# Kernel tuning notes

Measured on AMD Instinct MI355X. Metric: run time of the kernel, lower is better.

The kernel has to match this reference:

```python
import jax, jax.numpy as jnp
import numpy as np

B, T, D_IN, H, D_OUT = 64, 512, 256, 512, 1


def _lstm_layer(x, w_ih, w_hh, b_ih, b_hh):
    """PyTorch-convention LSTM layer. x: [B,T,Din]; w_ih: [4H,Din]; w_hh: [4H,H].
    Gate order: i, f, g, o. Zero initial h/c. Returns [B,T,H]."""
    h_dim = w_hh.shape[1]
    # Precompute input contribution for all timesteps: [B,T,4H]
    xg = jnp.einsum('bti,gi->btg', x, w_ih) + b_ih + b_hh
    xg = jnp.swapaxes(xg, 0, 1)  # [T,B,4H] for scan

    def step(carry, xg_t):
        h, c = carry
        gates = xg_t + h @ w_hh.T  # [B,4H]
        i, f, g, o = jnp.split(gates, 4, axis=-1)
        i = jax.nn.sigmoid(i)
        f = jax.nn.sigmoid(f)
        g = jnp.tanh(g)
        o = jax.nn.sigmoid(o)
        c = f * c + i * g
        h = o * jnp.tanh(c)
        return (h, c), h

    bsz = x.shape[0]
    h0 = jnp.zeros((bsz, h_dim), dtype=x.dtype)
    c0 = jnp.zeros((bsz, h_dim), dtype=x.dtype)
    _, hs = jax.lax.scan(step, (h0, c0), xg)  # hs: [T,B,H]
    return jnp.swapaxes(hs, 0, 1)  # [B,T,H]


def setup_inputs() -> dict:
    key = jax.random.key(0)
    ks = jax.random.split(key, 11)
    s_ih0 = 1.0 / np.sqrt(H)
    inp = {
        'x': jax.random.normal(ks[0], (B, T, D_IN), dtype=jnp.float32),
        'w_ih0': jax.random.uniform(ks[1], (4 * H, D_IN), jnp.float32, -s_ih0, s_ih0),
        'w_hh0': jax.random.uniform(ks[2], (4 * H, H), jnp.float32, -s_ih0, s_ih0),
        'b_ih0': jax.random.uniform(ks[3], (4 * H,), jnp.float32, -s_ih0, s_ih0),
        'b_hh0': jax.random.uniform(ks[4], (4 * H,), jnp.float32, -s_ih0, s_ih0),
        'w_ih1': jax.random.uniform(ks[5], (4 * H, H), jnp.float32, -s_ih0, s_ih0),
        'w_hh1': jax.random.uniform(ks[6], (4 * H, H), jnp.float32, -s_ih0, s_ih0),
        'b_ih1': jax.random.uniform(ks[7], (4 * H,), jnp.float32, -s_ih0, s_ih0),
        'b_hh1': jax.random.uniform(ks[8], (4 * H,), jnp.float32, -s_ih0, s_ih0),
        'w_fc': jax.random.uniform(ks[9], (D_OUT, H), jnp.float32, -s_ih0, s_ih0),
        'b_fc': jax.random.uniform(ks[10], (D_OUT,), jnp.float32, -s_ih0, s_ih0),
    }
    return inp


def reference(x, w_ih0, w_hh0, b_ih0, b_hh0, w_ih1, w_hh1, b_ih1, b_hh1, w_fc, b_fc):
    h = _lstm_layer(x, w_ih0, w_hh0, b_ih0, b_hh0)   # [B,T,H]
    h = _lstm_layer(h, w_ih1, w_hh1, b_ih1, b_hh1)   # [B,T,H]
    last = h[:, -1, :]                               # [B,H]
    logits = last @ w_fc.T + b_fc                    # [B,D_OUT]
    return jax.nn.sigmoid(logits)
```

## Files before the change

### kernel.cpp

```cpp
#include <hip/hip_runtime.h>
#include <stdint.h>
#include <stddef.h>

#define B_ 64
#define T_ 512
#define DIN 256
#define H_ 512
#define NWGF 128

typedef __attribute__((ext_vector_type(8))) short short8;
typedef __attribute__((ext_vector_type(4))) float f32x4;

__device__ __forceinline__ unsigned short f2bf(float f) {
  union { float f; unsigned u; } v; v.f = f;
  return (unsigned short)((v.u + 0x7fffu + ((v.u >> 16) & 1u)) >> 16);
}
__device__ __forceinline__ float bf2f(unsigned short s) {
  union { unsigned u; float f; } v; v.u = ((unsigned)s) << 16; return v.f;
}
__device__ __forceinline__ float sigmoidf_(float x) { return 1.f / (1.f + __expf(-x)); }
__device__ __forceinline__ float tanhf_(float x) { return 1.f - 2.f / (__expf(2.f * x) + 1.f); }

__device__ __forceinline__ void cohstore_u64(unsigned long long* p, unsigned long long v) {
  __hip_atomic_store(p, v, __ATOMIC_RELAXED, __HIP_MEMORY_SCOPE_AGENT);
}
__device__ __forceinline__ int cohload_i32(const int* p) {
  return __hip_atomic_load(p, __ATOMIC_RELAXED, __HIP_MEMORY_SCOPE_AGENT);
}
__device__ __forceinline__ void cohstore_i32(int* p, int v) {
  __hip_atomic_store(p, v, __ATOMIC_RELAXED, __HIP_MEMORY_SCOPE_AGENT);
}

__global__ void k_convert_x(const float* __restrict__ x, unsigned short* __restrict__ xT) {
  const int nq = T_ * B_ * DIN / 4;
  for (int q = blockIdx.x * blockDim.x + threadIdx.x; q < nq; q += gridDim.x * blockDim.x) {
    int e = q * 4;
    int d = e % DIN;
    int row = e / DIN;
    int b = row & (B_ - 1), t = row / B_;
    float4 v = *(const float4*)(x + ((size_t)b * T_ + t) * DIN + d);
    unsigned short o[4] = { f2bf(v.x), f2bf(v.y), f2bf(v.z), f2bf(v.w) };
    *(uint2*)(xT + (size_t)row * DIN + d) = *(const uint2*)o;
  }
}

__global__ __launch_bounds__(256, 1) void k_lstm8(
    const unsigned short* __restrict__ xT,
    const float* __restrict__ wih0, const float* __restrict__ whh0,
    const float* __restrict__ bih0, const float* __restrict__ bhh0,
    const float* __restrict__ wih1, const float* __restrict__ whh1,
    const float* __restrict__ bih1, const float* __restrict__ bhh1,
    unsigned short* __restrict__ h0, unsigned short* __restrict__ h1,
    int* __restrict__ flags0, int* __restrict__ flags1) {
  __shared__ unsigned short hbufA[16384];
  __shared__ unsigned short bufB[16384];
  __shared__ float gbuf[8 * 64 * 5];
  __shared__ unsigned short hstage[32 * 20];
  const int wgid = blockIdx.x;
  const int wg2 = wgid & 63;
  const int cg = wg2 >> 1, bh = wg2 & 1;
  const int tid = threadIdx.x;
  const int lane = tid & 63, wv = tid >> 6;
  const int l15 = lane & 15, l4 = lane >> 4;
  const int um = wv >> 1, rb = (wv & 1) * 2;
  const int colb = cg * 16, bb = bh * 32;

  if (wgid < 64) {
    short8 wih[8], whh[16];
    {
      const float* wr = wih0 + (size_t)(wv * H_ + colb + l15) * DIN + l4 * 8;
#pragma unroll
      for (int kk = 0; kk < 8; ++kk) {
        float4 v0 = *(const float4*)(wr + kk * 32);
        float4 v1 = *(const float4*)(wr + kk * 32 + 4);
        unsigned short o[8] = { f2bf(v0.x), f2bf(v0.y), f2bf(v0.z), f2bf(v0.w),
                                f2bf(v1.x), f2bf(v1.y), f2bf(v1.z), f2bf(v1.w) };
        wih[kk] = *(const short8*)o;
      }
      const float* wr2 = whh0 + (size_t)(wv * H_ + colb + l15) * H_ + l4 * 8;
#pragma unroll
      for (int kk = 0; kk < 16; ++kk) {
        float4 v0 = *(const float4*)(wr2 + kk * 32);
        float4 v1 = *(const float4*)(wr2 + kk * 32 + 4);
        unsigned short o[8] = { f2bf(v0.x), f2bf(v0.y), f2bf(v0.z), f2bf(v0.w),
                                f2bf(v1.x), f2bf(v1.y), f2bf(v1.z), f2bf(v1.w) };
        whh[kk] = *(const short8*)o;
      }
    }
    float b0s[4];
#pragma unroll
    for (int s = 0; s < 4; ++s)
      b0s[s] = bih0[s * H_ + colb + l15] + bhh0[s * H_ + colb + l15];
    float c2[2] = {0.f, 0.f};

    {
#pragma unroll
      for (int j = 0; j < 4; ++j) {
        int ch = tid + j * 256;
        int b = ch >> 5, g = ch & 31;
        uint4 v = *(const uint4*)(xT + (size_t)(bb + b) * DIN + g * 8);
        *(uint4*)&bufB[g * 256 + ((b ^ (g & 7)) * 8)] = v;
      }
    }
    __syncthreads();

    for (int t = 0; t < T_; ++t) {
      f32x4 aE[2] = {}, aO[2] = {};
      {
        const unsigned short* xb = bufB + (t & 1) * 8192;
#pragma unroll
        for (int kk = 0; kk < 8; kk += 2) {
          int g0 = kk * 4 + l4, g1 = (kk + 1) * 4 + l4;
#pragma unroll
          for (int m = 0; m < 2; ++m) {
            short8 a0 = *(const short8*)&xb[g0 * 256 + (((m * 16 + l15) ^ (g0 & 7)) * 8)];
            short8 a1 = *(const short8*)&xb[g1 * 256 + (((m * 16 + l15) ^ (g1 & 7)) * 8)];
            aE[m] = __builtin_amdgcn_mfma_f32_16x16x32_bf16(a0, wih[kk], aE[m], 0, 0, 0);
            aO[m] = __builtin_amdgcn_mfma_f32_16x16x32_bf16(a1, wih[kk + 1], aO[m], 0, 0, 0);
          }
        }
      }
      uint4 xv[4];
      const bool hasx = (t + 1 < T_);
      if (hasx) {
        const unsigned short* xs = xT + (size_t)(t + 1) * (B_ * DIN);
#pragma unroll
        for (int j = 0; j < 4; ++j) {
          int ch = tid + j * 256;
          xv[j] = *(const uint4*)(xs + (size_t)(bb + (ch >> 5)) * DIN + (ch & 31) * 8);
        }
      }
      if (t > 0) {
        for (;;) {
          int v = (lane < 32) ? cohload_i32(flags0 + (lane * 2 + bh) * 32) : 0x7fffffff;
          if (__all(v >= t)) break;
          __builtin_amdgcn_s_sleep(1);
        }
        __builtin_amdgcn_sched_barrier(0);
        asm volatile("" ::: "memory");
        const uint4* hp = (const uint4*)(h0 + ((size_t)(t - 1) * B_ + bb) * H_);
        uint4 tmp[8];
#pragma unroll
        for (int j = 0; j < 8; ++j) tmp[j] = hp[tid + j * 256];
#pragma unroll
        for (int j = 0; j < 8; ++j) {
          int ch = tid + j * 256;
          int b = ch >> 6, g = ch & 63;
          *(uint4*)&hbufA[g * 256 + ((b ^ (g & 7)) * 8)] = tmp[j];
        }
      }
      if (hasx) {
        unsigned short* xd = bufB + ((t + 1) & 1) * 8192;
#pragma unroll
        for (int j = 0; j < 4; ++j) {
          int ch = tid + j * 256;
          int b = ch >> 5, g = ch & 31;
          *(uint4*)&xd[g * 256 + ((b ^ (g & 7)) * 8)] = xv[j];
        }
      }
      __syncthreads();
      if (t > 0) {
#pragma unroll
        for (int kk = 0; kk < 16; kk += 2) {
          int g0 = kk * 4 + l4, g1 = (kk + 1) * 4 + l4;
#pragma unroll
          for (int m = 0; m < 2; ++m) {
            short8 a0 = *(const short8*)&hbufA[g0 * 256 + (((m * 16 + l15) ^ (g0 & 7)) * 8)];
            short8 a1 = *(const short8*)&hbufA[g1 * 256 + (((m * 16 + l15) ^ (g1 & 7)) * 8)];
            aE[m] = __builtin_amdgcn_mfma_f32_16x16x32_bf16(a0, whh[kk], aE[m], 0, 0, 0);
            aO[m] = __builtin_amdgcn_mfma_f32_16x16x32_bf16(a1, whh[kk + 1], aO[m], 0, 0, 0);
          }
        }
      }
#pragma unroll
      for (int m = 0; m < 2; ++m) {
        f32x4 acc = aE[m] + aO[m];
#pragma unroll
        for (int r = 0; r < 4; ++r)
          gbuf[((wv * 2 + m) * 64 + lane) * 5 + r] = acc[r];
      }
      __syncthreads();
#pragma unroll
      for (int rr = 0; rr < 2; ++rr) {
        int r = rb + rr;
        float g4[4];
#pragma unroll
        for (int s = 0; s < 4; ++s)
          g4[s] = gbuf[((s * 2 + um) * 64 + lane) * 5 + r] + b0s[s];
        float iv = sigmoidf_(g4[0]), fv = sigmoidf_(g4[1]);
        float gv = tanhf_(g4[2]), ov = sigmoidf_(g4[3]);
        float cn = fv * c2[rr] + iv * gv;
        c2[rr] = cn;
        hstage[(um * 16 + l4 * 4 + r) * 20 + l15] = f2bf(ov * tanhf_(cn));
      }
      __syncthreads();
      if (tid < 128) {
        int bl = tid >> 2, q = tid & 3;
        unsigned long long v = *(const unsigned long long*)&hstage[bl * 20 + q * 4];
        cohstore_u64((unsigned long long*)(h0 + ((size_t)t * B_ + bb + bl) * H_ + colb) + q, v);
      }
      asm volatile("s_waitcnt vmcnt(0)" ::: "memory");
      __syncthreads();
      if (tid == 0) cohstore_i32(flags0 + wg2 * 32, t + 1);
    }
  } else {
    short8 wA[16], wB[16];
    {
      const float* wrA = wih1 + (size_t)(wv * H_ + colb + l15) * H_ + l4 * 8;
      const float* wrB = whh1 + (size_t)(wv * H_ + colb + l15) * H_ + l4 * 8;
#pragma unroll
      for (int kk = 0; kk < 16; ++kk) {
        float4 a0 = *(const float4*)(wrA + kk * 32);
        float4 a1 = *(const float4*)(wrA + kk * 32 + 4);
        unsigned short oa[8] = { f2bf(a0.x), f2bf(a0.y), f2bf(a0.z), f2bf(a0.w),
                                 f2bf(a1.x), f2bf(a1.y), f2bf(a1.z), f2bf(a1.w) };
        wA[kk] = *(const short8*)oa;
        float4 b0 = *(const float4*)(wrB + kk * 32);
        float4 b1 = *(const float4*)(wrB + kk * 32 + 4);
        unsigned short ob[8] = { f2bf(b0.x), f2bf(b0.y), f2bf(b0.z), f2bf(b0.w),
                                 f2bf(b1.x), f2bf(b1.y), f2bf(b1.z), f2bf(b1.w) };
        wB[kk] = *(const short8*)ob;
      }
    }
    float b1s[4];
#pragma unroll
    for (int s = 0; s < 4; ++s)
      b1s[s] = bih1[s * H_ + colb + l15] + bhh1[s * H_ + colb + l15];
    float c2[2] = {0.f, 0.f};

    for (int t = 0; t < T_; ++t) {
      f32x4 aA[2] = {}, aB[2] = {};
      if (t > 0) {
        for (;;) {
          int v = (lane < 32) ? cohload_i32(flags1 + (lane * 2 + bh) * 32) : 0x7fffffff;
          if (__all(v >= t)) break;
          __builtin_amdgcn_s_sleep(1);
        }
        __builtin_amdgcn_sched_barrier(0);
        asm volatile("" ::: "memory");
        const uint4* hp = (const uint4*)(h1 + ((size_t)(t - 1) * B_ + bb) * H_);
        uint4 tmp[8];
#pragma unroll
        for (int j = 0; j < 8; ++j) tmp[j] = hp[tid + j * 256];
#pragma unroll
        for (int j = 0; j < 8; ++j) {
          int ch = tid + j * 256;
          int b = ch >> 6, g = ch & 63;
          *(uint4*)&bufB[g * 256 + ((b ^ (g & 7)) * 8)] = tmp[j];
        }
        __syncthreads();
#pragma unroll
        for (int kk = 0; kk < 16; ++kk) {
          int g = kk * 4 + l4;
#pragma unroll
          for (int m = 0; m < 2; ++m) {
            int e = g * 256 + (((m * 16 + l15) ^ (g & 7)) * 8);
            aB[m] = __builtin_amdgcn_mfma_f32_16x16x32_bf16(*(const short8*)&bufB[e], wB[kk], aB[m], 0, 0, 0);
          }
        }
      }
      for (;;) {
        int v = (lane < 32) ? cohload_i32(flags0 + (lane * 2 + bh) * 32) : 0x7fffffff;
        if (__all(v >= t + 1)) break;
        __builtin_amdgcn_s_sleep(1);
      }
      __builtin_amdgcn_sched_barrier(0);
      asm volatile("" ::: "memory");
      {
        const uint4* hp = (const uint4*)(h0 + ((size_t)t * B_ + bb) * H_);
        uint4 tmp[8];
#pragma unroll
        for (int j = 0; j < 8; ++j) tmp[j] = hp[tid + j * 256];
#pragma unroll
        for (int j = 0; j < 8; ++j) {
          int ch = tid + j * 256;
          int b = ch >> 6, g = ch & 63;
          *(uint4*)&hbufA[g * 256 + ((b ^ (g & 7)) * 8)] = tmp[j];
        }
      }
      __syncthreads();
#pragma unroll
      for (int kk = 0; kk < 16; ++kk) {
        int g = kk * 4 + l4;
#pragma unroll
        for (int m = 0; m < 2; ++m) {
          int e = g * 256 + (((m * 16 + l15) ^ (g & 7)) * 8);
          aA[m] = __builtin_amdgcn_mfma_f32_16x16x32_bf16(*(const short8*)&hbufA[e], wA[kk], aA[m], 0, 0, 0);
        }
      }
#pragma unroll
      for (int m = 0; m < 2; ++m) {
        f32x4 acc = aA[m] + aB[m];
#pragma unroll
        for (int r = 0; r < 4; ++r)
          gbuf[((wv * 2 + m) * 64 + lane) * 5 + r] = acc[r];
      }
      __syncthreads();
#pragma unroll
      for (int rr = 0; rr < 2; ++rr) {
        int r = rb + rr;
        float g4[4];
#pragma unroll
        for (int s = 0; s < 4; ++s)
          g4[s] = gbuf[((s * 2 + um) * 64 + lane) * 5 + r] + b1s[s];
        float iv = sigmoidf_(g4[0]), fv = sigmoidf_(g4[1]);
        float gv = tanhf_(g4[2]), ov = sigmoidf_(g4[3]);
        float cn = fv * c2[rr] + iv * gv;
        c2[rr] = cn;
        hstage[(um * 16 + l4 * 4 + r) * 20 + l15] = f2bf(ov * tanhf_(cn));
      }
      __syncthreads();
      if (tid < 128) {
        int bl = tid >> 2, q = tid & 3;
        unsigned long long v = *(const unsigned long long*)&hstage[bl * 20 + q * 4];
        cohstore_u64((unsigned long long*)(h1 + ((size_t)t * B_ + bb + bl) * H_ + colb) + q, v);
      }
      asm volatile("s_waitcnt vmcnt(0)" ::: "memory");
      __syncthreads();
      if (tid == 0) cohstore_i32(flags1 + wg2 * 32, t + 1);
    }
  }
}

__global__ void k_fc(const unsigned short* __restrict__ h1, const float* __restrict__ w,
                     const float* __restrict__ bfc, float* __restrict__ out) {
  int b = threadIdx.x;
  if (b < B_) {
    const unsigned short* hb = h1 + ((size_t)(T_ - 1) * B_ + b) * H_;
    float s = 0.f;
    for (int j = 0; j < H_; ++j) s += bf2f(hb[j]) * w[j];
    out[b] = sigmoidf_(s + bfc[0]);
  }
}

extern "C" void kernel_launch(void* const* d_in, const int* in_sizes, int n_in,
                              void* d_out, int out_size, void* d_ws, size_t ws_size,
                              hipStream_t stream) {
  (void)in_sizes; (void)n_in; (void)out_size; (void)ws_size;
  const float* x    = (const float*)d_in[0];
  const float* wih0 = (const float*)d_in[1];
  const float* whh0 = (const float*)d_in[2];
  const float* bih0 = (const float*)d_in[3];
  const float* bhh0 = (const float*)d_in[4];
  const float* wih1 = (const float*)d_in[5];
  const float* whh1 = (const float*)d_in[6];
  const float* bih1 = (const float*)d_in[7];
  const float* bhh1 = (const float*)d_in[8];
  const float* wfc  = (const float*)d_in[9];
  const float* bfc  = (const float*)d_in[10];
  float* out = (float*)d_out;

  const size_t HB = (size_t)T_ * B_ * H_ * 2;
  char* ws = (char*)d_ws;
  int* flags0 = (int*)ws;
  int* flags1 = (int*)(ws + 8192);
  unsigned short* h0 = (unsigned short*)(ws + 16384);
  unsigned short* h1 = (unsigned short*)(ws + 16384 + HB);
  unsigned short* xT = (unsigned short*)(ws + 16384 + 2 * HB);

  hipMemsetAsync(ws, 0, 16384, stream);
  k_convert_x<<<2048, 256, 0, stream>>>(x, xT);
  k_lstm8<<<NWGF, 256, 0, stream>>>(xT, wih0, whh0, bih0, bhh0,
                                    wih1, whh1, bih1, bhh1, h0, h1, flags0, flags1);
  k_fc<<<1, 64, 0, stream>>>(h1, wfc, bfc, out);
}
```

Measured before the change: 1.845 ms.

## Split batch into four 16-row groups across 256 persistent workgroups

Increases the persistent LSTM grid from 128 to 256 workgroups. Each workgroup now handles 16 batch rows instead of 32, so four independent batch groups per layer each synchronise only among their own 32 column workgroups. Per-step MFMA work, LDS traffic and gate work per workgroup are halved, with one gate per thread. Layer 1 now waits on layer 0's flags before its recurrent part and loads the layer-0 input earlier. The cost is more flag polling and global h traffic, and the workgroups must all be co-resident or the spin-waits can deadlock.

```diff
diff --git a/kernel.cpp b/kernel.cpp
--- a/kernel.cpp
+++ b/kernel.cpp
@@ -6,7 +6,7 @@
 #define T_ 512
 #define DIN 256
 #define H_ 512
-#define NWGF 128
+#define NWGF 256
 
 typedef __attribute__((ext_vector_type(8))) short short8;
 typedef __attribute__((ext_vector_type(4))) float f32x4;
@@ -44,28 +44,32 @@
   }
 }
 
-__global__ __launch_bounds__(256, 1) void k_lstm8(
+__global__ __launch_bounds__(256, 1) void k_lstm9(
     const unsigned short* __restrict__ xT,
     const float* __restrict__ wih0, const float* __restrict__ whh0,
     const float* __restrict__ bih0, const float* __restrict__ bhh0,
     const float* __restrict__ wih1, const float* __restrict__ whh1,
     const float* __restrict__ bih1, const float* __restrict__ bhh1,
     unsigned short* __restrict__ h0, unsigned short* __restrict__ h1,
-    int* __restrict__ flags0, int* __restrict__ flags1) {
-  __shared__ unsigned short hbufA[16384];
-  __shared__ unsigned short bufB[16384];
-  __shared__ float gbuf[8 * 64 * 5];
-  __shared__ unsigned short hstage[32 * 20];
-  const int wgid = blockIdx.x;
-  const int wg2 = wgid & 63;
-  const int cg = wg2 >> 1, bh = wg2 & 1;
+    int* __restrict__ flg) {
+  __shared__ unsigned short hbufA[8192];
+  __shared__ unsigned short bufB[8192];
+  __shared__ float gbuf[4 * 64 * 5];
+  __shared__ unsigned short hstage[16 * 20];
+  const int bid = blockIdx.x;
+  const int grp = bid & 7, cg = bid >> 3;
+  const int layer = grp >> 2, bq = grp & 3;
   const int tid = threadIdx.x;
   const int lane = tid & 63, wv = tid >> 6;
   const int l15 = lane & 15, l4 = lane >> 4;
-  const int um = wv >> 1, rb = (wv & 1) * 2;
-  const int colb = cg * 16, bb = bh * 32;
-
-  if (wgid < 64) {
+  const int colb = cg * 16, bb = bq * 16;
+  const int ucol = tid & 15, ubat = tid >> 4;
+  const int lp = (ubat >> 2) * 16 + ucol, ur = ubat & 3;
+  int* myflag = flg + (grp * 32 + cg) * 32;
+  const int* f_own = flg + (grp * 32) * 32;
+  const int* f_l0  = flg + (bq * 32) * 32;
+
+  if (layer == 0) {
     short8 wih[8], whh[16];
     {
       const float* wr = wih0 + (size_t)(wv * H_ + colb + l15) * DIN + l4 * 8;
@@ -90,72 +94,67 @@
     float b0s[4];
 #pragma unroll
     for (int s = 0; s < 4; ++s)
-      b0s[s] = bih0[s * H_ + colb + l15] + bhh0[s * H_ + colb + l15];
-    float c2[2] = {0.f, 0.f};
-
-    {
-#pragma unroll
-      for (int j = 0; j < 4; ++j) {
-        int ch = tid + j * 256;
-        int b = ch >> 5, g = ch & 31;
-        uint4 v = *(const uint4*)(xT + (size_t)(bb + b) * DIN + g * 8);
-        *(uint4*)&bufB[g * 256 + ((b ^ (g & 7)) * 8)] = v;
-      }
+      b0s[s] = bih0[s * H_ + colb + ucol] + bhh0[s * H_ + colb + ucol];
+    float cst = 0.f;
+
+#pragma unroll
+    for (int j = 0; j < 2; ++j) {
+      int ch = tid + j * 256;
+      int b = ch >> 5, g = ch & 31;
+      uint4 v = *(const uint4*)(xT + (size_t)(bb + b) * DIN + g * 8);
+      *(uint4*)&bufB[g * 128 + ((b ^ (g & 15)) * 8)] = v;
     }
     __syncthreads();
 
     for (int t = 0; t < T_; ++t) {
-      f32x4 aE[2] = {}, aO[2] = {};
+      f32x4 aE = {}, aO = {};
       {
-        const unsigned short* xb = bufB + (t & 1) * 8192;
+        const unsigned short* xb = bufB + (t & 1) * 4096;
 #pragma unroll
         for (int kk = 0; kk < 8; kk += 2) {
           int g0 = kk * 4 + l4, g1 = (kk + 1) * 4 + l4;
-#pragma unroll
-          for (int m = 0; m < 2; ++m) {
-            short8 a0 = *(const short8*)&xb[g0 * 256 + (((m * 16 + l15) ^ (g0 & 7)) * 8)];
-            short8 a1 = *(const short8*)&xb[g1 * 256 + (((m * 16 + l15) ^ (g1 & 7)) * 8)];
-            aE[m] = __builtin_amdgcn_mfma_f32_16x16x32_bf16(a0, wih[kk], aE[m], 0, 0, 0);
-            aO[m] = __builtin_amdgcn_mfma_f32_16x16x32_bf16(a1, wih[kk + 1], aO[m], 0, 0, 0);
-          }
-        }
-      }
-      uint4 xv[4];
+          short8 a0 = *(const short8*)&xb[g0 * 128 + ((l15 ^ (g0 & 15)) * 8)];
+          short8 a1 = *(const short8*)&xb[g1 * 128 + ((l15 ^ (g1 & 15)) * 8)];
+          aE = __builtin_amdgcn_mfma_f32_16x16x32_bf16(a0, wih[kk], aE, 0, 0, 0);
+          aO = __builtin_amdgcn_mfma_f32_16x16x32_bf16(a1, wih[kk + 1], aO, 0, 0, 0);
+        }
+      }
+      uint4 xv[2];
       const bool hasx = (t + 1 < T_);
       if (hasx) {
         const unsigned short* xs = xT + (size_t)(t + 1) * (B_ * DIN);
 #pragma unroll
-        for (int j = 0; j < 4; ++j) {
+        for (int j = 0; j < 2; ++j) {
           int ch = tid + j * 256;
           xv[j] = *(const uint4*)(xs + (size_t)(bb + (ch >> 5)) * DIN + (ch & 31) * 8);
         }
       }
       if (t > 0) {
         for (;;) {
-          int v = (lane < 32) ? cohload_i32(flags0 + (lane * 2 + bh) * 32) : 0x7fffffff;
+          int v = (lane < 32) ? cohload_i32(f_own + lane * 32) : 0x7fffffff;
           if (__all(v >= t)) break;
           __builtin_amdgcn_s_sleep(1);
         }
         __builtin_amdgcn_sched_barrier(0);
         asm volatile("" ::: "memory");
         const uint4* hp = (const uint4*)(h0 + ((size_t)(t - 1) * B_ + bb) * H_);
-        uint4 tmp[8];
-#pragma unroll
-        for (int j = 0; j < 8; ++j) tmp[j] = hp[tid + j * 256];
-#pragma unroll
-        for (int j = 0; j < 8; ++j) {
+        uint4 tmp[4];
+#pragma unroll
+        for (int j = 0; j < 4; ++j) tmp[j] = hp[tid + j * 256];
+#pragma unroll
+        for (int j = 0; j < 4; ++j) {
           int ch = tid + j * 256;
           int b = ch >> 6, g = ch & 63;
-          *(uint4*)&hbufA[g * 256 + ((b ^ (g & 7)) * 8)] = tmp[j];
+          *(uint4*)&hbufA[g * 128 + ((b ^ (g & 15)) * 8)] = tmp[j];
         }
       }
       if (hasx) {
-        unsigned short* xd = bufB + ((t + 1) & 1) * 8192;
-#pragma unroll
-        for (int j = 0; j < 4; ++j) {
+        unsigned short* xd = bufB + ((t + 1) & 1) * 4096;
+#pragma unroll
+        for (int j = 0; j < 2; ++j) {
           int ch = tid + j * 256;
           int b = ch >> 5, g = ch & 31;
-          *(uint4*)&xd[g * 256 + ((b ^ (g & 7)) * 8)] = xv[j];
+          *(uint4*)&xd[g * 128 + ((b ^ (g & 15)) * 8)] = xv[j];
         }
       }
       __syncthreads();
@@ -163,45 +162,34 @@
 #pragma unroll
         for (int kk = 0; kk < 16; kk += 2) {
           int g0 = kk * 4 + l4, g1 = (kk + 1) * 4 + l4;
-#pragma unroll
-          for (int m = 0; m < 2; ++m) {
-            short8 a0 = *(const short8*)&hbufA[g0 * 256 + (((m * 16 + l15) ^ (g0 & 7)) * 8)];
-            short8 a1 = *(const short8*)&hbufA[g1 * 256 + (((m * 16 + l15) ^ (g1 & 7)) * 8)];
-            aE[m] = __builtin_amdgcn_mfma_f32_16x16x32_bf16(a0, whh[kk], aE[m], 0, 0, 0);
-            aO[m] = __builtin_amdgcn_mfma_f32_16x16x32_bf16(a1, whh[kk + 1], aO[m], 0, 0, 0);
-          }
-        }
-      }
-#pragma unroll
-      for (int m = 0; m < 2; ++m) {
-        f32x4 acc = aE[m] + aO[m];
-#pragma unroll
-        for (int r = 0; r < 4; ++r)
-          gbuf[((wv * 2 + m) * 64 + lane) * 5 + r] = acc[r];
-      }
-      __syncthreads();
-#pragma unroll
-      for (int rr = 0; rr < 2; ++rr) {
-        int r = rb + rr;
+          short8 a0 = *(const short8*)&hbufA[g0 * 128 + ((l15 ^ (g0 & 15)) * 8)];
+          short8 a1 = *(const short8*)&hbufA[g1 * 128 + ((l15 ^ (g1 & 15)) * 8)];
+          aE = __builtin_amdgcn_mfma_f32_16x16x32_bf16(a0, whh[kk], aE, 0, 0, 0);
+          aO = __builtin_amdgcn_mfma_f32_16x16x32_bf16(a1, whh[kk + 1], aO, 0, 0, 0);
+        }
+      }
+      f32x4 acc = aE + aO;
+#pragma unroll
+      for (int r = 0; r < 4; ++r) gbuf[(wv * 64 + lane) * 5 + r] = acc[r];
+      __syncthreads();
+      {
         float g4[4];
 #pragma unroll
-        for (int s = 0; s < 4; ++s)
-          g4[s] = gbuf[((s * 2 + um) * 64 + lane) * 5 + r] + b0s[s];
+        for (int s = 0; s < 4; ++s) g4[s] = gbuf[(s * 64 + lp) * 5 + ur] + b0s[s];
         float iv = sigmoidf_(g4[0]), fv = sigmoidf_(g4[1]);
         float gv = tanhf_(g4[2]), ov = sigmoidf_(g4[3]);
-        float cn = fv * c2[rr] + iv * gv;
-        c2[rr] = cn;
-        hstage[(um * 16 + l4 * 4 + r) * 20 + l15] = f2bf(ov * tanhf_(cn));
-      }
-      __syncthreads();
-      if (tid < 128) {
+        cst = fv * cst + iv * gv;
+        hstage[ubat * 20 + ucol] = f2bf(ov * tanhf_(cst));
+      }
+      __syncthreads();
+      if (tid < 64) {
         int bl = tid >> 2, q = tid & 3;
         unsigned long long v = *(const unsigned long long*)&hstage[bl * 20 + q * 4];
         cohstore_u64((unsigned long long*)(h0 + ((size_t)t * B_ + bb + bl) * H_ + colb) + q, v);
       }
       asm volatile("s_waitcnt vmcnt(0)" ::: "memory");
       __syncthreads();
-      if (tid == 0) cohstore_i32(flags0 + wg2 * 32, t + 1);
+      if (tid == 0) cohstore_i32(myflag, t + 1);
     }
   } else {
     short8 wA[16], wB[16];
@@ -225,99 +213,92 @@
     float b1s[4];
 #pragma unroll
     for (int s = 0; s < 4; ++s)
-      b1s[s] = bih1[s * H_ + colb + l15] + bhh1[s * H_ + colb + l15];
-    float c2[2] = {0.f, 0.f};
+      b1s[s] = bih1[s * H_ + colb + ucol] + bhh1[s * H_ + colb + ucol];
+    float cst = 0.f;
 
     for (int t = 0; t < T_; ++t) {
-      f32x4 aA[2] = {}, aB[2] = {};
+      for (;;) {
+        int v = (lane < 32) ? cohload_i32(f_l0 + lane * 32) : 0x7fffffff;
+        if (__all(v >= t + 1)) break;
+        __builtin_amdgcn_s_sleep(1);
+      }
+      __builtin_amdgcn_sched_barrier(0);
+      asm volatile("" ::: "memory");
+      uint4 ha[4];
+      {
+        const uint4* hp = (const uint4*)(h0 + ((size_t)t * B_ + bb) * H_);
+#pragma unroll
+        for (int j = 0; j < 4; ++j) ha[j] = hp[tid + j * 256];
+      }
       if (t > 0) {
         for (;;) {
-          int v = (lane < 32) ? cohload_i32(flags1 + (lane * 2 + bh) * 32) : 0x7fffffff;
+          int v = (lane < 32) ? cohload_i32(f_own + lane * 32) : 0x7fffffff;
           if (__all(v >= t)) break;
           __builtin_amdgcn_s_sleep(1);
         }
         __builtin_amdgcn_sched_barrier(0);
         asm volatile("" ::: "memory");
         const uint4* hp = (const uint4*)(h1 + ((size_t)(t - 1) * B_ + bb) * H_);
-        uint4 tmp[8];
-#pragma unroll
-        for (int j = 0; j < 8; ++j) tmp[j] = hp[tid + j * 256];
-#pragma unroll
-        for (int j = 0; j < 8; ++j) {
+        uint4 hbv[4];
+#pragma unroll
+        for (int j = 0; j < 4; ++j) hbv[j] = hp[tid + j * 256];
+#pragma unroll
+        for (int j = 0; j < 4; ++j) {
           int ch = tid + j * 256;
           int b = ch >> 6, g = ch & 63;
-          *(uint4*)&bufB[g * 256 + ((b ^ (g & 7)) * 8)] = tmp[j];
-        }
-        __syncthreads();
-#pragma unroll
-        for (int kk = 0; kk < 16; ++kk) {
-          int g = kk * 4 + l4;
-#pragma unroll
-          for (int m = 0; m < 2; ++m) {
-            int e = g * 256 + (((m * 16 + l15) ^ (g & 7)) * 8);
-            aB[m] = __builtin_amdgcn_mfma_f32_16x16x32_bf16(*(const short8*)&bufB[e], wB[kk], aB[m], 0, 0, 0);
-          }
-        }
-      }
-      for (;;) {
-        int v = (lane < 32) ? cohload_i32(flags0 + (lane * 2 + bh) * 32) : 0x7fffffff;
-        if (__all(v >= t + 1)) break;
-        __builtin_amdgcn_s_sleep(1);
-      }
-      __builtin_amdgcn_sched_barrier(0);
-      asm volatile("" ::: "memory");
+          *(uint4*)&bufB[g * 128 + ((b ^ (g & 15)) * 8)] = hbv[j];
+        }
+      }
+      __syncthreads();
+      f32x4 bE = {}, bO = {};
+      if (t > 0) {
+#pragma unroll
+        for (int kk = 0; kk < 16; kk += 2) {
+          int g0 = kk * 4 + l4, g1 = (kk + 1) * 4 + l4;
+          short8 a0 = *(const short8*)&bufB[g0 * 128 + ((l15 ^ (g0 & 15)) * 8)];
+          short8 a1 = *(const short8*)&bufB[g1 * 128 + ((l15 ^ (g1 & 15)) * 8)];
+          bE = __builtin_amdgcn_mfma_f32_16x16x32_bf16(a0, wB[kk], bE, 0, 0, 0);
+          bO = __builtin_amdgcn_mfma_f32_16x16x32_bf16(a1, wB[kk + 1], bO, 0, 0, 0);
+        }
+      }
+#pragma unroll
+      for (int j = 0; j < 4; ++j) {
+        int ch = tid + j * 256;
+        int b = ch >> 6, g = ch & 63;
+        *(uint4*)&hbufA[g * 128 + ((b ^ (g & 15)) * 8)] = ha[j];
+      }
+      __syncthreads();
+      f32x4 aE = {}, aO = {};
+#pragma unroll
+      for (int kk = 0; kk < 16; kk += 2) {
+        int g0 = kk * 4 + l4, g1 = (kk + 1) * 4 + l4;
+        short8 a0 = *(const short8*)&hbufA[g0 * 128 + ((l15 ^ (g0 & 15)) * 8)];
+        short8 a1 = *(const short8*)&hbufA[g1 * 128 + ((l15 ^ (g1 & 15)) * 8)];
+        aE = __builtin_amdgcn_mfma_f32_16x16x32_bf16(a0, wA[kk], aE, 0, 0, 0);
+        aO = __builtin_amdgcn_mfma_f32_16x16x32_bf16(a1, wA[kk + 1], aO, 0, 0, 0);
+      }
+      f32x4 acc = (aE + aO) + (bE + bO);
+#pragma unroll
+      for (int r = 0; r < 4; ++r) gbuf[(wv * 64 + lane) * 5 + r] = acc[r];
+      __syncthreads();
       {
-        const uint4* hp = (const uint4*)(h0 + ((size_t)t * B_ + bb) * H_);
-        uint4 tmp[8];
-#pragma unroll
-        for (int j = 0; j < 8; ++j) tmp[j] = hp[tid + j * 256];
-#pragma unroll
-        for (int j = 0; j < 8; ++j) {
-          int ch = tid + j * 256;
-          int b = ch >> 6, g = ch & 63;
-          *(uint4*)&hbufA[g * 256 + ((b ^ (g & 7)) * 8)] = tmp[j];
-        }
-      }
-      __syncthreads();
-#pragma unroll
-      for (int kk = 0; kk < 16; ++kk) {
-        int g = kk * 4 + l4;
-#pragma unroll
-        for (int m = 0; m < 2; ++m) {
-          int e = g * 256 + (((m * 16 + l15) ^ (g & 7)) * 8);
-          aA[m] = __builtin_amdgcn_mfma_f32_16x16x32_bf16(*(const short8*)&hbufA[e], wA[kk], aA[m], 0, 0, 0);
-        }
-      }
-#pragma unroll
-      for (int m = 0; m < 2; ++m) {
-        f32x4 acc = aA[m] + aB[m];
-#pragma unroll
-        for (int r = 0; r < 4; ++r)
-          gbuf[((wv * 2 + m) * 64 + lane) * 5 + r] = acc[r];
-      }
-      __syncthreads();
-#pragma unroll
-      for (int rr = 0; rr < 2; ++rr) {
-        int r = rb + rr;
         float g4[4];
 #pragma unroll
-        for (int s = 0; s < 4; ++s)
-          g4[s] = gbuf[((s * 2 + um) * 64 + lane) * 5 + r] + b1s[s];
+        for (int s = 0; s < 4; ++s) g4[s] = gbuf[(s * 64 + lp) * 5 + ur] + b1s[s];
         float iv = sigmoidf_(g4[0]), fv = sigmoidf_(g4[1]);
         float gv = tanhf_(g4[2]), ov = sigmoidf_(g4[3]);
-        float cn = fv * c2[rr] + iv * gv;
-        c2[rr] = cn;
-        hstage[(um * 16 + l4 * 4 + r) * 20 + l15] = f2bf(ov * tanhf_(cn));
-      }
-      __syncthreads();
-      if (tid < 128) {
+        cst = fv * cst + iv * gv;
+        hstage[ubat * 20 + ucol] = f2bf(ov * tanhf_(cst));
+      }
+      __syncthreads();
+      if (tid < 64) {
         int bl = tid >> 2, q = tid & 3;
         unsigned long long v = *(const unsigned long long*)&hstage[bl * 20 + q * 4];
         cohstore_u64((unsigned long long*)(h1 + ((size_t)t * B_ + bb + bl) * H_ + colb) + q, v);
       }
       asm volatile("s_waitcnt vmcnt(0)" ::: "memory");
       __syncthreads();
-      if (tid == 0) cohstore_i32(flags1 + wg2 * 32, t + 1);
+      if (tid == 0) cohstore_i32(myflag, t + 1);
     }
   }
 }
@@ -352,15 +333,14 @@
 
   const size_t HB = (size_t)T_ * B_ * H_ * 2;
   char* ws = (char*)d_ws;
-  int* flags0 = (int*)ws;
-  int* flags1 = (int*)(ws + 8192);
-  unsigned short* h0 = (unsigned short*)(ws + 16384);
-  unsigned short* h1 = (unsigned short*)(ws + 16384 + HB);
-  unsigned short* xT = (unsigned short*)(ws + 16384 + 2 * HB);
-
-  hipMemsetAsync(ws, 0, 16384, stream);
+  int* flg = (int*)ws;
+  unsigned short* h0 = (unsigned short*)(ws + 32768);
+  unsigned short* h1 = (unsigned short*)(ws + 32768 + HB);
+  unsigned short* xT = (unsigned short*)(ws + 32768 + 2 * HB);
+
+  hipMemsetAsync(ws, 0, 32768, stream);
   k_convert_x<<<2048, 256, 0, stream>>>(x, xT);
-  k_lstm8<<<NWGF, 256, 0, stream>>>(xT, wih0, whh0, bih0, bhh0,
-                                    wih1, whh1, bih1, bhh1, h0, h1, flags0, flags1);
+  k_lstm9<<<NWGF, 256, 0, stream>>>(xT, wih0, whh0, bih0, bhh0,
+                                    wih1, whh1, bih1, bhh1, h0, h1, flg);
   k_fc<<<1, 64, 0, stream>>>(h1, wfc, bfc, out);
 }
```

New measurement: 1.842 ms. No clear change (-0.2%).
